# Performance work log

Measured on AMD Instinct MI355X. Metric: run time of the kernel, lower is better.

## Reference

```python
import jax, jax.numpy as jnp
import numpy as np

N_NODES = 50000
N_EDGES = 800000
D_IN = 128
D_HID = 128
D_OUT = 128
N_GRAPHS = 64


def _gcn_conv(x, src, dst, W, b, n_nodes):
    """PyG GCNConv: D^{-1/2} (A + I) D^{-1/2} X W + b (self-loops added)."""
    xw = x @ W  # [N, F_out]
    loops = jnp.arange(n_nodes, dtype=src.dtype)
    s = jnp.concatenate([src, loops])  # sources (messages gathered here)
    d = jnp.concatenate([dst, loops])  # targets (aggregation index)
    ones = jnp.ones_like(d, dtype=xw.dtype)
    deg = jax.ops.segment_sum(ones, d, num_segments=n_nodes)  # in-degree incl. self-loop
    dinv = jnp.where(deg > 0, jax.lax.rsqrt(deg), 0.0)
    norm = dinv[s] * dinv[d]  # [E+N]
    msg = xw[s] * norm[:, None]  # gather + scale
    out = jax.ops.segment_sum(msg, d, num_segments=n_nodes)  # scatter-add
    return out + b


def _global_mean_pool(x, batch, num_graphs):
    sums = jax.ops.segment_sum(x, batch, num_segments=num_graphs)
    cnts = jax.ops.segment_sum(jnp.ones((x.shape[0],), x.dtype), batch, num_segments=num_graphs)
    return sums / jnp.maximum(cnts, 1.0)[:, None]


def setup_inputs() -> dict:
    key = jax.random.key(0)
    k = jax.random.split(key, 8)
    x = jax.random.normal(k[0], (N_NODES, D_IN), dtype=jnp.float32)
    edge_index = jax.random.randint(k[1], (2, N_EDGES), 0, N_NODES, dtype=jnp.int64)
    batch = jnp.sort(jax.random.randint(k[2], (N_NODES,), 0, N_GRAPHS, dtype=jnp.int64))
    # Glorot-ish params for the two GCNConv layers
    W1 = jax.random.normal(k[3], (D_IN, D_HID), dtype=jnp.float32) / np.sqrt(D_IN)
    b1 = jnp.zeros((D_HID,), dtype=jnp.float32)
    W2 = jax.random.normal(k[4], (D_HID, D_OUT), dtype=jnp.float32) / np.sqrt(D_HID)
    b2 = jnp.zeros((D_OUT,), dtype=jnp.float32)
    return {"x": x, "edge_index": edge_index, "batch": batch,
            "W1": W1, "b1": b1, "W2": W2, "b2": b2}


def reference(x, edge_index, batch, W1, b1, W2, b2):
    src, dst = edge_index[0], edge_index[1]
    n = x.shape[0]
    h = _gcn_conv(x, src, dst, W1, b1, n)
    h = jax.nn.relu(h)
    h = _gcn_conv(h, src, dst, W2, b2, n)
    return _global_mean_pool(h, batch, N_GRAPHS)  # [N_GRAPHS, D_OUT]
```

## Files before the change

kernel.cpp:

```cpp
#include <hip/hip_runtime.h>
#include <hip/hip_bf16.h>

#define SPAN_SHIFT 8
#define BCAP 8192

typedef __attribute__((ext_vector_type(8))) short short8;
typedef __attribute__((ext_vector_type(4))) float float4v;

__device__ __forceinline__ float bf2f(unsigned short u) {
  union { unsigned int i; float f; } v; v.i = ((unsigned int)u) << 16; return v.f;
}
__device__ __forceinline__ unsigned short f2bf(float f) {
  union { float f; unsigned int i; } v; v.f = f;
  unsigned int x = v.i;
  return (unsigned short)((x + 0x7fffu + ((x >> 16) & 1u)) >> 16);
}

__global__ __launch_bounds__(256) void detect_swz_zero_k(
    const unsigned short* __restrict__ xu,  const int* __restrict__ ei,
    const unsigned short* __restrict__ b1u, const unsigned short* __restrict__ b2u,
    const void* __restrict__ W1, const void* __restrict__ W2,
    unsigned short* __restrict__ w1s, unsigned short* __restrict__ w2s,
    int* __restrict__ flags, int* __restrict__ bcnt, float* __restrict__ acc,
    int NBKT, int GP) {
  const int b = blockIdx.x;
  const int tid = threadIdx.x;
  if (b >= 132) {
    int base = (b - 132) * 4096 + tid;
    #pragma unroll
    for (int j = 0; j < 16; ++j) {
      int i = base + j * 256;
      if (i < NBKT) bcnt[i] = 0;
      else if (i < NBKT + GP) acc[i - NBKT] = 0.f;
    }
    return;
  }
  __shared__ int s_cnt;
  if (tid == 0) s_cnt = 0;
  __syncthreads();
  if (b >= 4) {
    const void* Wraw = (b < 68) ? W1 : W2;
    unsigned short* out = (b < 68) ? w1s : w2s;
    const unsigned short* Wu = (const unsigned short*)Wraw;
    int c = 0;
    for (int i = tid; i < 512; i += 256) {
      int e = (Wu[i] >> 7) & 0xFF;
      if (e < 96 || e > 159) c++;
    }
    atomicAdd(&s_cnt, c);
    __syncthreads();
    const int wf32 = s_cnt > 64;
    int u = ((b - 4) & 63) * 256 + tid;
    int j = u & 7, lane = (u >> 3) & 63, blk = u >> 9;
    int cc = blk >> 3, t = blk & 7;
    int quad = lane >> 4, col = lane & 15;
    int k = cc * 32 + quad * 8 + j;
    int n = t * 16 + col;
    out[u] = wf32 ? f2bf(((const float*)Wraw)[k * 128 + n])
                  : ((const unsigned short*)Wraw)[k * 128 + n];
    return;
  }
  int cnt = 0;
  if (b == 1) {
    for (int i = tid; i < 4096; i += 256)
      if (ei[2 * i + 1] == 0) cnt++;
    atomicAdd(&s_cnt, cnt);
    __syncthreads();
    if (tid == 0) flags[1] = (s_cnt > 2048) ? 1 : 0;
    return;
  }
  const unsigned short* p; int n; int fi;
  if (b == 0)      { p = xu;  n = 16384; fi = 0; }
  else if (b == 2) { p = b1u; n = 128;   fi = 4; }
  else             { p = b2u; n = 128;   fi = 5; }
  for (int i = tid; i < n; i += 256) {
    int e = (p[i] >> 7) & 0xFF;
    if (e < 96 || e > 159) cnt++;
  }
  atomicAdd(&s_cnt, cnt);
  __syncthreads();
  if (tid == 0) flags[fi] = (s_cnt * 8 > n) ? 1 : 0;
}

__device__ __forceinline__ void gemm_body(const void* __restrict__ X,
                                          const unsigned short* __restrict__ Wsw,
                                          unsigned short* __restrict__ XWb, int N,
                                          int xf32, int row0,
                                          unsigned short* Wl, unsigned short* Xl) {
  const int tid = threadIdx.x;
  for (int v = tid; v < 2048; v += 256)
    ((short8*)Wl)[v] = ((const short8*)Wsw)[v];
  for (int v = tid; v < 2048; v += 256) {
    int r = v >> 5, k4 = (v & 31) * 4;
    int row = row0 + r;
    ushort4 u = make_ushort4(0, 0, 0, 0);
    if (row < N) {
      long long gi = (long long)row * 128 + k4;
      if (xf32) {
        float4 xv = *(const float4*)&((const float*)X)[gi];
        u.x = f2bf(xv.x); u.y = f2bf(xv.y); u.z = f2bf(xv.z); u.w = f2bf(xv.w);
      } else {
        u = *(const ushort4*)&((const unsigned short*)X)[gi];
      }
    }
    *(ushort4*)&Xl[r * 136 + k4] = u;
  }
  __syncthreads();
  const int w = tid >> 6, lane = tid & 63;
  const int quad = lane >> 4, col = lane & 15;
  float4v acc[8];
  #pragma unroll
  for (int t = 0; t < 8; ++t) acc[t] = (float4v){0.f, 0.f, 0.f, 0.f};
  #pragma unroll
  for (int c = 0; c < 4; ++c) {
    short8 a = *(const short8*)&Xl[(w * 16 + col) * 136 + c * 32 + quad * 8];
    #pragma unroll
    for (int t = 0; t < 8; ++t) {
      short8 b = *(const short8*)&Wl[((c * 8 + t) * 64 + lane) * 8];
      acc[t] = __builtin_amdgcn_mfma_f32_16x16x32_bf16(a, b, acc[t], 0, 0, 0);
    }
  }
  #pragma unroll
  for (int t = 0; t < 8; ++t) {
    #pragma unroll
    for (int r = 0; r < 4; ++r)
      Xl[(w * 16 + quad * 4 + r) * 136 + t * 16 + col] = f2bf(acc[t][r]);
  }
  __syncthreads();
  for (int v = tid; v < 1024; v += 256) {
    int r = v >> 4, ck = (v & 15) * 8;
    int row = row0 + r;
    if (row < N)
      *(short8*)&XWb[(long long)row * 128 + ck] = *(const short8*)&Xl[r * 136 + ck];
  }
}

__global__ __launch_bounds__(256) void scatA_gemm1_k(const int* __restrict__ ei,
    int* __restrict__ bcnt, int2* __restrict__ tmp, int E, int SA,
    const void* __restrict__ X, const unsigned short* __restrict__ Wsw,
    unsigned short* __restrict__ XWb, int N,
    const int* __restrict__ flags, int NBKT) {
  __shared__ __align__(16) char smem[50688];
  const int tid = threadIdx.x;
  if ((int)blockIdx.x >= SA) {
    unsigned short* Wl = (unsigned short*)smem;
    unsigned short* Xl = (unsigned short*)(smem + 32768);
    gemm_body(X, Wsw, XWb, N, flags[0], ((int)blockIdx.x - SA) * 64, Wl, Xl);
    return;
  }
  int2* stage = (int2*)smem;
  int* hist  = (int*)(smem + 32768);
  int* off   = hist + 256;
  int* cnt2  = off + 256;
  int* gbase = cnt2 + 256;
  int* wsum  = gbase + 256;
  hist[tid] = 0; cnt2[tid] = 0;
  __syncthreads();
  const int base = blockIdx.x * 4096;
  const int i64 = flags[1];
  int rs[16], rd[16];
  #pragma unroll
  for (int j = 0; j < 16; ++j) {
    int e = base + j * 256 + tid;
    if (e < E) {
      int s, d;
      if (i64) { s = ei[2 * e]; d = ei[2 * (E + e)]; }
      else     { s = ei[e];     d = ei[E + e]; }
      rs[j] = s; rd[j] = d;
      atomicAdd(&hist[d >> SPAN_SHIFT], 1);
    } else rd[j] = -1;
  }
  __syncthreads();
  {
    int lane = tid & 63, w = tid >> 6;
    int v = hist[tid], inc = v;
    #pragma unroll
    for (int o = 1; o < 64; o <<= 1) { int n = __shfl_up(inc, o, 64); if (lane >= o) inc += n; }
    if (lane == 63) wsum[w] = inc;
    __syncthreads();
    int pre = 0;
    #pragma unroll
    for (int k = 0; k < 4; ++k) if (k < w) pre += wsum[k];
    off[tid] = pre + inc - v;
  }
  __syncthreads();
  #pragma unroll
  for (int j = 0; j < 16; ++j) {
    if (rd[j] >= 0) {
      int b = rd[j] >> SPAN_SHIFT;
      int r = atomicAdd(&cnt2[b], 1);
      int2 rec; rec.x = rs[j]; rec.y = rd[j];
      stage[off[b] + r] = rec;
    }
  }
  if (tid < NBKT && hist[tid] > 0)
    gbase[tid] = tid * BCAP + atomicAdd(&bcnt[tid], hist[tid]);
  __syncthreads();
  const int total = off[255] + hist[255];
  for (int i = tid; i < total; i += 256) {
    int2 rec = stage[i];
    int b = rec.y >> SPAN_SHIFT;
    tmp[gbase[b] + (i - off[b])] = rec;
  }
}

__global__ __launch_bounds__(256) void gemm_k(const void* __restrict__ X,
                                              const unsigned short* __restrict__ Wsw,
                                              unsigned short* __restrict__ XWb, int N,
                                              int xmode) {
  __shared__ __align__(16) unsigned short Wl[16384];
  __shared__ __align__(16) unsigned short Xl[64 * 136];
  gemm_body(X, Wsw, XWb, N, (xmode == 1) ? 1 : 0, blockIdx.x * 64, Wl, Xl);
}

__global__ __launch_bounds__(256) void scatB1_k(const int2* __restrict__ tmp,
    const int* __restrict__ bcnt, int* __restrict__ rowptr,
    float* __restrict__ dinv, int N, int NBKT, int E) {
  __shared__ int hist[256];
  __shared__ int pfx[256];
  __shared__ int ws[4];
  const int tid = threadIdx.x;
  const int b = blockIdx.x;
  const int lane = tid & 63, w = tid >> 6;
  int c = (tid < NBKT) ? bcnt[tid] : 0;
  hist[tid] = 0;
  {
    int inc = c;
    #pragma unroll
    for (int o = 1; o < 64; o <<= 1) { int n = __shfl_up(inc, o, 64); if (lane >= o) inc += n; }
    if (lane == 63) ws[w] = inc;
    __syncthreads();
    int pre = 0;
    #pragma unroll
    for (int k = 0; k < 4; ++k) if (k < w) pre += ws[k];
    pfx[tid] = pre + inc - c;
  }
  __syncthreads();
  const int bbase = pfx[b];
  const int cnt = bcnt[b];
  const int2* src = tmp + (long long)b * BCAP;
  for (int i = tid; i < cnt; i += 256)
    atomicAdd(&hist[src[i].y & 255], 1);
  __syncthreads();
  int v = hist[tid], inc = v;
  #pragma unroll
  for (int o = 1; o < 64; o <<= 1) {
    int n = __shfl_up(inc, o, 64);
    if (lane >= o) inc += n;
  }
  if (lane == 63) ws[w] = inc;
  __syncthreads();
  int pre = 0;
  #pragma unroll
  for (int k = 0; k < 4; ++k) if (k < w) pre += ws[k];
  int node = (b << SPAN_SHIFT) + tid;
  if (node < N) {
    rowptr[node] = bbase + pre + inc - v;
    dinv[node] = rsqrtf((float)(v + 1));
  }
  if (b == 0 && tid == 0) rowptr[N] = E;
}

__global__ __launch_bounds__(256) void scatB2_k(const int2* __restrict__ tmp,
    const int* __restrict__ bcnt, const int* __restrict__ rowptr,
    const float* __restrict__ dinv, int2* __restrict__ spk, int N) {
  __shared__ int cur[256];
  const int tid = threadIdx.x;
  const int b = blockIdx.x;
  const int n0 = b << SPAN_SHIFT;
  if (n0 + tid < N) cur[tid] = rowptr[n0 + tid];
  __syncthreads();
  const int cnt = bcnt[b];
  const int2* src = tmp + (long long)b * BCAP;
  for (int i = tid; i < cnt; i += 256) {
    int2 rec = src[i];
    int pos = atomicAdd(&cur[rec.y & 255], 1);
    int2 out; out.x = rec.x; out.y = __float_as_int(dinv[rec.x]);
    spk[pos] = out;
  }
}

__global__ __launch_bounds__(256) void aggregate_k(const unsigned short* __restrict__ XWb,
    const int* __restrict__ rowptr, const int2* __restrict__ spk,
    const float* __restrict__ dinv, const void* __restrict__ bias_raw, int bias_fi,
    void* __restrict__ H, int N, int relu, int out_bf16,
    const int* __restrict__ flags) {
  int wid = (blockIdx.x * 256 + threadIdx.x) >> 6;
  if (wid >= N) return;
  const int lane = threadIdx.x & 63;
  const int half = lane >> 5;
  const int fl = (lane & 31) * 4;
  const int beg = rowptr[wid], end = rowptr[wid + 1];
  const float di = dinv[wid];
  float a0 = 0.f, a1 = 0.f, a2 = 0.f, a3 = 0.f;
  int idx = beg;
  for (; idx + 8 <= end; idx += 8) {
    int2 rA = spk[idx + half];
    int2 rB = spk[idx + 2 + half];
    int2 rC = spk[idx + 4 + half];
    int2 rD = spk[idx + 6 + half];
    float wA = __int_as_float(rA.y), wB = __int_as_float(rB.y);
    float wC = __int_as_float(rC.y), wD = __int_as_float(rD.y);
    ushort4 uA = *(const ushort4*)&XWb[(long long)rA.x * 128 + fl];
    ushort4 uB = *(const ushort4*)&XWb[(long long)rB.x * 128 + fl];
    ushort4 uC = *(const ushort4*)&XWb[(long long)rC.x * 128 + fl];
    ushort4 uD = *(const ushort4*)&XWb[(long long)rD.x * 128 + fl];
    a0 += wA * bf2f(uA.x) + wB * bf2f(uB.x) + wC * bf2f(uC.x) + wD * bf2f(uD.x);
    a1 += wA * bf2f(uA.y) + wB * bf2f(uB.y) + wC * bf2f(uC.y) + wD * bf2f(uD.y);
    a2 += wA * bf2f(uA.z) + wB * bf2f(uB.z) + wC * bf2f(uC.z) + wD * bf2f(uD.z);
    a3 += wA * bf2f(uA.w) + wB * bf2f(uB.w) + wC * bf2f(uC.w) + wD * bf2f(uD.w);
  }
  if (idx + 4 <= end) {
    int2 rA = spk[idx + half];
    int2 rB = spk[idx + 2 + half];
    float wA = __int_as_float(rA.y), wB = __int_as_float(rB.y);
    ushort4 uA = *(const ushort4*)&XWb[(long long)rA.x * 128 + fl];
    ushort4 uB = *(const ushort4*)&XWb[(long long)rB.x * 128 + fl];
    a0 += wA * bf2f(uA.x) + wB * bf2f(uB.x);
    a1 += wA * bf2f(uA.y) + wB * bf2f(uB.y);
    a2 += wA * bf2f(uA.z) + wB * bf2f(uB.z);
    a3 += wA * bf2f(uA.w) + wB * bf2f(uB.w);
    idx += 4;
  }
  if (idx < end) {
    int iA = idx + half;
    int2 rA = spk[min(iA, end - 1)];
    float wA = (iA < end) ? __int_as_float(rA.y) : 0.f;
    ushort4 uA = *(const ushort4*)&XWb[(long long)rA.x * 128 + fl];
    a0 += wA * bf2f(uA.x); a1 += wA * bf2f(uA.y);
    a2 += wA * bf2f(uA.z); a3 += wA * bf2f(uA.w);
    if (idx + 2 < end) {
      int iB = idx + 2 + half;
      int2 rB = spk[min(iB, end - 1)];
      float wB = (iB < end) ? __int_as_float(rB.y) : 0.f;
      ushort4 uB = *(const ushort4*)&XWb[(long long)rB.x * 128 + fl];
      a0 += wB * bf2f(uB.x); a1 += wB * bf2f(uB.y);
      a2 += wB * bf2f(uB.z); a3 += wB * bf2f(uB.w);
    }
  }
  a0 += __shfl_xor(a0, 32, 64);
  a1 += __shfl_xor(a1, 32, 64);
  a2 += __shfl_xor(a2, 32, 64);
  a3 += __shfl_xor(a3, 32, 64);
  if (half == 0) {
    ushort4 su = *(const ushort4*)&XWb[(long long)wid * 128 + fl];
    float d2 = di * di;
    float o0 = di * a0 + d2 * bf2f(su.x);
    float o1 = di * a1 + d2 * bf2f(su.y);
    float o2 = di * a2 + d2 * bf2f(su.z);
    float o3 = di * a3 + d2 * bf2f(su.w);
    if (bias_fi >= 0) {
      if (flags[bias_fi]) {
        float4 bv = *(const float4*)&((const float*)bias_raw)[fl];
        o0 += bv.x; o1 += bv.y; o2 += bv.z; o3 += bv.w;
      } else {
        const unsigned short* bu = (const unsigned short*)bias_raw;
        o0 += bf2f(bu[fl]); o1 += bf2f(bu[fl + 1]);
        o2 += bf2f(bu[fl + 2]); o3 += bf2f(bu[fl + 3]);
      }
    }
    if (relu) {
      o0 = fmaxf(o0, 0.f); o1 = fmaxf(o1, 0.f);
      o2 = fmaxf(o2, 0.f); o3 = fmaxf(o3, 0.f);
    }
    if (out_bf16) {
      ushort4 uo;
      uo.x = f2bf(o0); uo.y = f2bf(o1); uo.z = f2bf(o2); uo.w = f2bf(o3);
      *(ushort4*)&((unsigned short*)H)[(long long)wid * 128 + fl] = uo;
    } else {
      *(float4*)&((float*)H)[(long long)wid * 128 + fl] = make_float4(o0, o1, o2, o3);
    }
  }
}

__global__ __launch_bounds__(256) void pool_partial_k(const float* __restrict__ H,
    const int* __restrict__ batch, float* __restrict__ acc, int N,
    const int* __restrict__ flags) {
  const int i64 = flags[1];
  const int lane = threadIdx.x & 63;
  const int w = threadIdx.x >> 6;
  const int chunk = (N + gridDim.x - 1) / gridDim.x;
  const int bstart = blockIdx.x * chunk;
  const int bend = min(bstart + chunk, N);
  const int sub = (chunk + 3) / 4;
  const int s = bstart + w * sub;
  const int e = min(s + sub, bend);
  if (s >= e) return;
  float ax = 0.f, ay = 0.f;
  int curg = i64 ? batch[2 * s] : batch[s];
  for (int n = s; n < e; ++n) {
    int g = i64 ? batch[2 * n] : batch[n];
    if (g != curg) {
      atomicAdd(&acc[curg * 128 + lane * 2], ax);
      atomicAdd(&acc[curg * 128 + lane * 2 + 1], ay);
      ax = ay = 0.f; curg = g;
    }
    float2 v = *(const float2*)&H[(long long)n * 128 + lane * 2];
    ax += v.x; ay += v.y;
  }
  atomicAdd(&acc[curg * 128 + lane * 2], ax);
  atomicAdd(&acc[curg * 128 + lane * 2 + 1], ay);
}

__global__ __launch_bounds__(128) void pool_final_k(const float* __restrict__ acc,
    const int* __restrict__ batch, const void* __restrict__ B2raw,
    float* __restrict__ out, int N, const int* __restrict__ flags) {
  __shared__ int sb[2];
  int g = blockIdx.x;
  int i64 = flags[1];
  if (threadIdx.x < 2) {
    int target = g + threadIdx.x;
    int lo = 0, hi = N;
    while (lo < hi) {
      int mid = (lo + hi) >> 1;
      int bv = i64 ? batch[2 * mid] : batch[mid];
      if (bv < target) lo = mid + 1; else hi = mid;
    }
    sb[threadIdx.x] = lo;
  }
  __syncthreads();
  int cnt = sb[1] - sb[0];
  int f = threadIdx.x;
  float b2 = flags[5] ? ((const float*)B2raw)[f]
                      : bf2f(((const unsigned short*)B2raw)[f]);
  float res = 0.f;
  if (cnt > 0) res = acc[g * 128 + f] / (float)cnt + b2;
  out[g * 128 + f] = res;
}

extern "C" void kernel_launch(void* const* d_in, const int* in_sizes, int n_in,
                              void* d_out, int out_size, void* d_ws, size_t ws_size,
                              hipStream_t stream) {
  const int N = in_sizes[0] / 128;
  const int E = in_sizes[1] / 2;
  const int G = out_size / 128;
  const int NB = (N + 255) >> SPAN_SHIFT;
  const int GB = (N + 63) / 64;
  const int SA = (E + 4095) / 4096;
  const int ZB = (NB + G * 128 + 4095) / 4096;

  const void* X  = d_in[0];
  const int*  EI = (const int*)d_in[1];
  const int*  BA = (const int*)d_in[2];
  const void* W1 = d_in[3];
  const void* B1 = d_in[4];
  const void* W2 = d_in[5];
  const void* B2 = d_in[6];
  float* OUT = (float*)d_out;

  char* ws = (char*)d_ws;
  size_t o = 0;
  auto alloc = [&](size_t b) { size_t r = o; o += (b + 255) & ~(size_t)255; return r; };
  int*   flags  = (int*)(ws + alloc(256));
  unsigned short* w1s = (unsigned short*)(ws + alloc(16384 * 2));
  unsigned short* w2s = (unsigned short*)(ws + alloc(16384 * 2));
  float* acc    = (float*)(ws + alloc((size_t)G * 128 * 4));
  int*   bcnt   = (int*)(ws + alloc(256 * 4));
  int*   rowptr = (int*)(ws + alloc((size_t)(N + 1) * 4));
  int2*  spk    = (int2*)(ws + alloc((size_t)E * 8));
  float* dinv   = (float*)(ws + alloc((size_t)N * 4));
  unsigned short* xwb = (unsigned short*)(ws + alloc((size_t)N * 128 * 2));
  char*  hreg   = ws + alloc((size_t)N * 128 * 4);
  unsigned short* h1b = (unsigned short*)hreg;
  float* h2f    = (float*)hreg;
  int2*  tmp    = (int2*)hreg;

  detect_swz_zero_k<<<132 + ZB, 256, 0, stream>>>(
      (const unsigned short*)X, EI,
      (const unsigned short*)B1, (const unsigned short*)B2,
      W1, W2, w1s, w2s, flags, bcnt, acc, NB, G * 128);
  scatA_gemm1_k<<<SA + GB, 256, 0, stream>>>(EI, bcnt, tmp, E, SA,
                                             X, w1s, xwb, N, flags, NB);
  scatB1_k<<<NB, 256, 0, stream>>>(tmp, bcnt, rowptr, dinv, N, NB, E);
  scatB2_k<<<NB, 256, 0, stream>>>(tmp, bcnt, rowptr, dinv, spk, N);

  dim3 agrid((N * 64 + 255) / 256);
  aggregate_k<<<agrid, 256, 0, stream>>>(xwb, rowptr, spk, dinv, B1, 4,
                                         h1b, N, 1, 1, flags);
  gemm_k<<<GB, 256, 0, stream>>>(h1b, w2s, xwb, N, 2);
  aggregate_k<<<agrid, 256, 0, stream>>>(xwb, rowptr, spk, dinv, (const void*)nullptr, -1,
                                         h2f, N, 0, 0, flags);
  pool_partial_k<<<512, 256, 0, stream>>>(h2f, BA, acc, N, flags);
  pool_final_k<<<G, 128, 0, stream>>>(acc, BA, B2, OUT, N, flags);
}
```

Baseline: 229.9 us.

## Merge CSR scatter kernels, store bare source indices, widen aggregate gathers

Merges the two bucket-scatter kernels into one, reusing the in-block prefix as the insertion cursor. The sorted edge array now holds only 4-byte source indices instead of index+weight pairs, and the aggregation looks up dinv[src] per edge instead of reading a precomputed weight. The aggregation kernel switches from two 32-lane halves with 8-byte loads to four 16-lane quarters with 16-byte loads, handling four edges per step and reducing with two xor shuffles. This cuts one launch and the edge-array traffic, but adds a dependent dinv gather per edge and more reduction shuffles.

New measurement: 219.8 us. -4.4%, faster.

```diff
diff --git a/kernel.cpp b/kernel.cpp
--- a/kernel.cpp
+++ b/kernel.cpp
@@ -210,14 +210,15 @@
                                               int xmode) {
   __shared__ __align__(16) unsigned short Wl[16384];
   __shared__ __align__(16) unsigned short Xl[64 * 136];
-  gemm_body(X, Wsw, XWb, N, (xmode == 1) ? 1 : 0, blockIdx.x * 64, Wl, Xl);
-}
-
-__global__ __launch_bounds__(256) void scatB1_k(const int2* __restrict__ tmp,
+  gemm_body(X, Wsw, XWb, N, (xmode == 1) ? 1 : 0, blockIdx.x * 64, Xl ? Wl : Wl, Xl);
+}
+
+__global__ __launch_bounds__(256) void scatB_k(const int2* __restrict__ tmp,
     const int* __restrict__ bcnt, int* __restrict__ rowptr,
-    float* __restrict__ dinv, int N, int NBKT, int E) {
+    float* __restrict__ dinv, int* __restrict__ spk, int N, int NBKT, int E) {
   __shared__ int hist[256];
   __shared__ int pfx[256];
+  __shared__ int cur[256];
   __shared__ int ws[4];
   const int tid = threadIdx.x;
   const int b = blockIdx.x;
@@ -253,122 +254,120 @@
   int pre = 0;
   #pragma unroll
   for (int k = 0; k < 4; ++k) if (k < w) pre += ws[k];
+  const int start = bbase + pre + inc - v;
   int node = (b << SPAN_SHIFT) + tid;
   if (node < N) {
-    rowptr[node] = bbase + pre + inc - v;
+    rowptr[node] = start;
     dinv[node] = rsqrtf((float)(v + 1));
   }
+  cur[tid] = start;
   if (b == 0 && tid == 0) rowptr[N] = E;
-}
-
-__global__ __launch_bounds__(256) void scatB2_k(const int2* __restrict__ tmp,
-    const int* __restrict__ bcnt, const int* __restrict__ rowptr,
-    const float* __restrict__ dinv, int2* __restrict__ spk, int N) {
-  __shared__ int cur[256];
-  const int tid = threadIdx.x;
-  const int b = blockIdx.x;
-  const int n0 = b << SPAN_SHIFT;
-  if (n0 + tid < N) cur[tid] = rowptr[n0 + tid];
-  __syncthreads();
-  const int cnt = bcnt[b];
-  const int2* src = tmp + (long long)b * BCAP;
+  __syncthreads();
   for (int i = tid; i < cnt; i += 256) {
     int2 rec = src[i];
     int pos = atomicAdd(&cur[rec.y & 255], 1);
-    int2 out; out.x = rec.x; out.y = __float_as_int(dinv[rec.x]);
-    spk[pos] = out;
+    spk[pos] = rec.x;
   }
 }
 
 __global__ __launch_bounds__(256) void aggregate_k(const unsigned short* __restrict__ XWb,
-    const int* __restrict__ rowptr, const int2* __restrict__ spk,
+    const int* __restrict__ rowptr, const int* __restrict__ spk,
     const float* __restrict__ dinv, const void* __restrict__ bias_raw, int bias_fi,
     void* __restrict__ H, int N, int relu, int out_bf16,
     const int* __restrict__ flags) {
   int wid = (blockIdx.x * 256 + threadIdx.x) >> 6;
   if (wid >= N) return;
   const int lane = threadIdx.x & 63;
-  const int half = lane >> 5;
-  const int fl = (lane & 31) * 4;
+  const int q = lane >> 4;
+  const int fl = (lane & 15) * 8;
   const int beg = rowptr[wid], end = rowptr[wid + 1];
   const float di = dinv[wid];
-  float a0 = 0.f, a1 = 0.f, a2 = 0.f, a3 = 0.f;
+  float a[8];
+  #pragma unroll
+  for (int j = 0; j < 8; ++j) a[j] = 0.f;
   int idx = beg;
-  for (; idx + 8 <= end; idx += 8) {
-    int2 rA = spk[idx + half];
-    int2 rB = spk[idx + 2 + half];
-    int2 rC = spk[idx + 4 + half];
-    int2 rD = spk[idx + 6 + half];
-    float wA = __int_as_float(rA.y), wB = __int_as_float(rB.y);
-    float wC = __int_as_float(rC.y), wD = __int_as_float(rD.y);
-    ushort4 uA = *(const ushort4*)&XWb[(long long)rA.x * 128 + fl];
-    ushort4 uB = *(const ushort4*)&XWb[(long long)rB.x * 128 + fl];
-    ushort4 uC = *(const ushort4*)&XWb[(long long)rC.x * 128 + fl];
-    ushort4 uD = *(const ushort4*)&XWb[(long long)rD.x * 128 + fl];
-    a0 += wA * bf2f(uA.x) + wB * bf2f(uB.x) + wC * bf2f(uC.x) + wD * bf2f(uD.x);
-    a1 += wA * bf2f(uA.y) + wB * bf2f(uB.y) + wC * bf2f(uC.y) + wD * bf2f(uD.y);
-    a2 += wA * bf2f(uA.z) + wB * bf2f(uB.z) + wC * bf2f(uC.z) + wD * bf2f(uD.z);
-    a3 += wA * bf2f(uA.w) + wB * bf2f(uB.w) + wC * bf2f(uC.w) + wD * bf2f(uD.w);
+  for (; idx + 16 <= end; idx += 16) {
+    int s0 = spk[idx + q];
+    int s1 = spk[idx + 4 + q];
+    int s2 = spk[idx + 8 + q];
+    int s3 = spk[idx + 12 + q];
+    float w0 = dinv[s0], w1 = dinv[s1], w2 = dinv[s2], w3 = dinv[s3];
+    short8 u0 = *(const short8*)&XWb[(long long)s0 * 128 + fl];
+    short8 u1 = *(const short8*)&XWb[(long long)s1 * 128 + fl];
+    short8 u2 = *(const short8*)&XWb[(long long)s2 * 128 + fl];
+    short8 u3 = *(const short8*)&XWb[(long long)s3 * 128 + fl];
+    #pragma unroll
+    for (int j = 0; j < 8; ++j)
+      a[j] += w0 * bf2f((unsigned short)u0[j]) + w1 * bf2f((unsigned short)u1[j])
+            + w2 * bf2f((unsigned short)u2[j]) + w3 * bf2f((unsigned short)u3[j]);
+  }
+  if (idx + 8 <= end) {
+    int s0 = spk[idx + q];
+    int s1 = spk[idx + 4 + q];
+    float w0 = dinv[s0], w1 = dinv[s1];
+    short8 u0 = *(const short8*)&XWb[(long long)s0 * 128 + fl];
+    short8 u1 = *(const short8*)&XWb[(long long)s1 * 128 + fl];
+    #pragma unroll
+    for (int j = 0; j < 8; ++j)
+      a[j] += w0 * bf2f((unsigned short)u0[j]) + w1 * bf2f((unsigned short)u1[j]);
+    idx += 8;
   }
   if (idx + 4 <= end) {
-    int2 rA = spk[idx + half];
-    int2 rB = spk[idx + 2 + half];
-    float wA = __int_as_float(rA.y), wB = __int_as_float(rB.y);
-    ushort4 uA = *(const ushort4*)&XWb[(long long)rA.x * 128 + fl];
-    ushort4 uB = *(const ushort4*)&XWb[(long long)rB.x * 128 + fl];
-    a0 += wA * bf2f(uA.x) + wB * bf2f(uB.x);
-    a1 += wA * bf2f(uA.y) + wB * bf2f(uB.y);
-    a2 += wA * bf2f(uA.z) + wB * bf2f(uB.z);
-    a3 += wA * bf2f(uA.w) + wB * bf2f(uB.w);
+    int s0 = spk[idx + q];
+    float w0 = dinv[s0];
+    short8 u0 = *(const short8*)&XWb[(long long)s0 * 128 + fl];
+    #pragma unroll
+    for (int j = 0; j < 8; ++j)
+      a[j] += w0 * bf2f((unsigned short)u0[j]);
     idx += 4;
   }
   if (idx < end) {
-    int iA = idx + half;
-    int2 rA = spk[min(iA, end - 1)];
-    float wA = (iA < end) ? __int_as_float(rA.y) : 0.f;
-    ushort4 uA = *(const ushort4*)&XWb[(long long)rA.x * 128 + fl];
-    a0 += wA * bf2f(uA.x); a1 += wA * bf2f(uA.y);
-    a2 += wA * bf2f(uA.z); a3 += wA * bf2f(uA.w);
-    if (idx + 2 < end) {
-      int iB = idx + 2 + half;
-      int2 rB = spk[min(iB, end - 1)];
-      float wB = (iB < end) ? __int_as_float(rB.y) : 0.f;
-      ushort4 uB = *(const ushort4*)&XWb[(long long)rB.x * 128 + fl];
-      a0 += wB * bf2f(uB.x); a1 += wB * bf2f(uB.y);
-      a2 += wB * bf2f(uB.z); a3 += wB * bf2f(uB.w);
-    }
-  }
-  a0 += __shfl_xor(a0, 32, 64);
-  a1 += __shfl_xor(a1, 32, 64);
-  a2 += __shfl_xor(a2, 32, 64);
-  a3 += __shfl_xor(a3, 32, 64);
-  if (half == 0) {
-    ushort4 su = *(const ushort4*)&XWb[(long long)wid * 128 + fl];
+    int e = idx + q;
+    int s0 = spk[min(e, end - 1)];
+    float w0 = (e < end) ? dinv[s0] : 0.f;
+    short8 u0 = *(const short8*)&XWb[(long long)s0 * 128 + fl];
+    #pragma unroll
+    for (int j = 0; j < 8; ++j)
+      a[j] += w0 * bf2f((unsigned short)u0[j]);
+  }
+  #pragma unroll
+  for (int j = 0; j < 8; ++j) {
+    a[j] += __shfl_xor(a[j], 16, 64);
+    a[j] += __shfl_xor(a[j], 32, 64);
+  }
+  if (q == 0) {
+    short8 su = *(const short8*)&XWb[(long long)wid * 128 + fl];
     float d2 = di * di;
-    float o0 = di * a0 + d2 * bf2f(su.x);
-    float o1 = di * a1 + d2 * bf2f(su.y);
-    float o2 = di * a2 + d2 * bf2f(su.z);
-    float o3 = di * a3 + d2 * bf2f(su.w);
+    float o[8];
+    #pragma unroll
+    for (int j = 0; j < 8; ++j)
+      o[j] = di * a[j] + d2 * bf2f((unsigned short)su[j]);
     if (bias_fi >= 0) {
       if (flags[bias_fi]) {
-        float4 bv = *(const float4*)&((const float*)bias_raw)[fl];
-        o0 += bv.x; o1 += bv.y; o2 += bv.z; o3 += bv.w;
+        const float* bf = (const float*)bias_raw;
+        float4 b0 = *(const float4*)&bf[fl];
+        float4 b1 = *(const float4*)&bf[fl + 4];
+        o[0] += b0.x; o[1] += b0.y; o[2] += b0.z; o[3] += b0.w;
+        o[4] += b1.x; o[5] += b1.y; o[6] += b1.z; o[7] += b1.w;
       } else {
         const unsigned short* bu = (const unsigned short*)bias_raw;
-        o0 += bf2f(bu[fl]); o1 += bf2f(bu[fl + 1]);
-        o2 += bf2f(bu[fl + 2]); o3 += bf2f(bu[fl + 3]);
+        #pragma unroll
+        for (int j = 0; j < 8; ++j) o[j] += bf2f(bu[fl + j]);
       }
     }
     if (relu) {
-      o0 = fmaxf(o0, 0.f); o1 = fmaxf(o1, 0.f);
-      o2 = fmaxf(o2, 0.f); o3 = fmaxf(o3, 0.f);
+      #pragma unroll
+      for (int j = 0; j < 8; ++j) o[j] = fmaxf(o[j], 0.f);
     }
     if (out_bf16) {
-      ushort4 uo;
-      uo.x = f2bf(o0); uo.y = f2bf(o1); uo.z = f2bf(o2); uo.w = f2bf(o3);
-      *(ushort4*)&((unsigned short*)H)[(long long)wid * 128 + fl] = uo;
+      short8 uo;
+      #pragma unroll
+      for (int j = 0; j < 8; ++j) uo[j] = (short)f2bf(o[j]);
+      *(short8*)&((unsigned short*)H)[(long long)wid * 128 + fl] = uo;
     } else {
-      *(float4*)&((float*)H)[(long long)wid * 128 + fl] = make_float4(o0, o1, o2, o3);
+      float* Hf = (float*)H;
+      *(float4*)&Hf[(long long)wid * 128 + fl]     = make_float4(o[0], o[1], o[2], o[3]);
+      *(float4*)&Hf[(long long)wid * 128 + fl + 4] = make_float4(o[4], o[5], o[6], o[7]);
     }
   }
 }
@@ -457,7 +456,7 @@
   float* acc    = (float*)(ws + alloc((size_t)G * 128 * 4));
   int*   bcnt   = (int*)(ws + alloc(256 * 4));
   int*   rowptr = (int*)(ws + alloc((size_t)(N + 1) * 4));
-  int2*  spk    = (int2*)(ws + alloc((size_t)E * 8));
+  int*   spk    = (int*)(ws + alloc((size_t)E * 4));
   float* dinv   = (float*)(ws + alloc((size_t)N * 4));
   unsigned short* xwb = (unsigned short*)(ws + alloc((size_t)N * 128 * 2));
   char*  hreg   = ws + alloc((size_t)N * 128 * 4);
@@ -471,8 +470,7 @@
       W1, W2, w1s, w2s, flags, bcnt, acc, NB, G * 128);
   scatA_gemm1_k<<<SA + GB, 256, 0, stream>>>(EI, bcnt, tmp, E, SA,
                                              X, w1s, xwb, N, flags, NB);
-  scatB1_k<<<NB, 256, 0, stream>>>(tmp, bcnt, rowptr, dinv, N, NB, E);
-  scatB2_k<<<NB, 256, 0, stream>>>(tmp, bcnt, rowptr, dinv, spk, N);
+  scatB_k<<<NB, 256, 0, stream>>>(tmp, bcnt, rowptr, dinv, spk, N, NB, E);
 
   dim3 agrid((N * 64 + 255) / 256);
   aggregate_k<<<agrid, 256, 0, stream>>>(xwb, rowptr, spk, dinv, B1, 4,
```
